# Kernel tuning notes

Hardware: AMD Instinct MI355X
Metric: run time of the kernel (lower is better)

The kernel has to match this reference:

```python
import jax, jax.numpy as jnp
import numpy as np

B, C, V = 1024, 512, 256  # batch, num_conjunctions, num_variables


def setup_inputs() -> dict:
    key = jax.random.key(0)
    k1, k2, k3 = jax.random.split(key, 3)
    x0 = jax.random.uniform(k1, (B, V), dtype=jnp.float32)
    # torch init: conj = 1 - 2*rand  -> uniform in (-1, 1)
    conjunctions = 1.0 - 2.0 * jax.random.uniform(k2, (C, 2 * V), dtype=jnp.float32)
    # rw = 10 - 20*rand -> uniform in (-10, 10)
    rule_weights = 10.0 - 20.0 * jax.random.uniform(k3, (C,), dtype=jnp.float32)
    return {"x0": x0, "conjunctions": conjunctions, "rule_weights": rule_weights}


def reference(x0, conjunctions, rule_weights):
    mu = jax.nn.sigmoid(conjunctions)            # (C, 2V)
    x = jnp.concatenate((x0, 1.0 - x0), axis=1)  # (B, 2V)
    # fuzzy-AND: broadcast mul-add then min over literal axis
    x_pot = mu[None, :, :] * x[:, None, :] + (1.0 - mu)[None, :, :]  # (B, C, 2V)
    fit = jnp.min(x_pot, axis=-1)                # (B, C)
    return 5.0 + jnp.sum(rule_weights * fit, axis=-1)  # (B,)
```

## Files before the change

kernel.cpp:

```cpp
#include <hip/hip_runtime.h>


#define B_    1024
#define C_    512
#define V_    256
#define TWOV  512

#define BPB    8
#define NBG    (B_ / BPB)
#define NCH    2

typedef float    f32x4 __attribute__((ext_vector_type(4)));
typedef _Float16 h16x2 __attribute__((ext_vector_type(2)));

__device__ __forceinline__ float sigf(float z) {
    return 1.0f / (1.0f + __expf(-z));
}
__device__ __forceinline__ float packh2(float a, float b) {
    h16x2 h; h.x = (_Float16)a; h.y = (_Float16)b;
    return __builtin_bit_cast(float, h);
}

#define PKMUL(D, A, Bq) asm("v_pk_mul_f16 %0, %1, %2" : "=v"(D) : "v"(A), "v"(Bq))
#define PKMAX(ACC, T)   asm("v_pk_max_f16 %0, %0, %1" : "+v"(ACC) : "v"(T))

__global__ __launch_bounds__(512) void k_prep(const float* __restrict__ conj,
                                              float4* __restrict__ muH,
                                              float* __restrict__ out) {
    const int vq = blockIdx.x;
    const int c  = threadIdx.x;
    if (vq < 2) out[vq * 512 + c] = 5.0f;
    const float* row = conj + (size_t)c * TWOV;
    const int v = vq * 4;
    float4 r;
    r.x = packh2(sigf(row[v + 0]),      sigf(row[v + 1]));
    r.y = packh2(sigf(row[v + 2]),      sigf(row[v + 3]));
    r.z = packh2(sigf(row[V_ + v + 0]), sigf(row[V_ + v + 1]));
    r.w = packh2(sigf(row[V_ + v + 2]), sigf(row[V_ + v + 3]));
    muH[(size_t)vq * C_ + c] = r;
}

__global__ __launch_bounds__(512, 2) void k_main(const float* __restrict__ x0,
                                                 const float4* __restrict__ muH,
                                                 const float* __restrict__ rw,
                                                 float* __restrict__ out) {
    const int tid  = threadIdx.x;
    const int lane = tid & 63;
    const int wave = tid >> 6;
    const int bg   = blockIdx.x;
    const int chunk= blockIdx.y;
    const int cA   = chunk * 256 + lane;
    const int vq0  = wave * 8;

    __shared__ float4 xs4[BPB * 64];
    __shared__ float  red[8 * 64 * 17];

    {
        const int b = tid >> 6, vq = tid & 63;
        float4 xv = *reinterpret_cast<const float4*>(
            x0 + (size_t)(bg * BPB + b) * V_ + vq * 4);
        float4 pk;
        pk.x = packh2(xv.x, xv.y);
        pk.y = packh2(xv.z, xv.w);
        pk.z = packh2(1.0f - xv.x, 1.0f - xv.y);
        pk.w = packh2(1.0f - xv.z, 1.0f - xv.w);
        xs4[tid] = pk;
    }

    const float4* p = muH + (size_t)vq0 * C_ + cA;

    float accA[BPB], accB[BPB], accC[BPB], accD[BPB];
#pragma unroll
    for (int i = 0; i < BPB; ++i) {
        accA[i] = 0.0f; accB[i] = 0.0f; accC[i] = 0.0f; accD[i] = 0.0f;
    }

    float4 MA = p[0];
    float4 MB = p[64];
    float4 MC = p[128];
    float4 MD = p[192];

    __syncthreads();

#define CPIECE(XC, M, ACC) do { \
    float t0, t1, t2, t3; \
    PKMUL(t0, M.x, XC.z);    \
    PKMUL(t1, M.z, XC.x);    \
    PKMUL(t2, M.y, XC.w);    \
    PKMUL(t3, M.w, XC.y);    \
    PKMAX(ACC, t0); PKMAX(ACC, t1); PKMAX(ACC, t2); PKMAX(ACC, t3); \
    } while (0)

#define PAIR4(XC, bi) do { \
    CPIECE(XC, MA, accA[bi]); \
    CPIECE(XC, MB, accB[bi]); \
    CPIECE(XC, MC, accC[bi]); \
    CPIECE(XC, MD, accD[bi]); \
    } while (0)

#pragma unroll
    for (int q = 0; q < 8; ++q) {
        float4 xc0 = xs4[0 * 64 + vq0 + q];
        float4 xc1 = xs4[1 * 64 + vq0 + q];
        float4 xc2 = xs4[2 * 64 + vq0 + q];
        float4 xc3 = xs4[3 * 64 + vq0 + q];
        float4 xc4 = xs4[4 * 64 + vq0 + q];
        float4 xc5 = xs4[5 * 64 + vq0 + q];
        float4 xc6 = xs4[6 * 64 + vq0 + q];
        float4 xc7 = xs4[7 * 64 + vq0 + q];
        float4 NA, NB, NC, ND;
        if (q < 7) {
            NA = p[(size_t)(q + 1) * C_];
            NB = p[(size_t)(q + 1) * C_ + 64];
            NC = p[(size_t)(q + 1) * C_ + 128];
            ND = p[(size_t)(q + 1) * C_ + 192];
        }
        asm volatile("" : "+v"(MA.x), "+v"(MA.y), "+v"(MA.z), "+v"(MA.w),
                          "+v"(MB.x), "+v"(MB.y), "+v"(MB.z), "+v"(MB.w),
                          "+v"(MC.x), "+v"(MC.y), "+v"(MC.z), "+v"(MC.w),
                          "+v"(MD.x), "+v"(MD.y), "+v"(MD.z), "+v"(MD.w));
        PAIR4(xc0, 0);
        PAIR4(xc1, 1);
        PAIR4(xc2, 2);
        PAIR4(xc3, 3);
        PAIR4(xc4, 4);
        PAIR4(xc5, 5);
        PAIR4(xc6, 6);
        PAIR4(xc7, 7);
        if (q < 7) { MA = NA; MB = NB; MC = NC; MD = ND; }
    }
#undef PAIR4
#undef CPIECE

    float mA[BPB], mB[BPB], mC[BPB], mD[BPB];
#pragma unroll
    for (int bi = 0; bi < BPB; ++bi) {
        h16x2 ha = __builtin_bit_cast(h16x2, accA[bi]);
        h16x2 hb = __builtin_bit_cast(h16x2, accB[bi]);
        h16x2 hc = __builtin_bit_cast(h16x2, accC[bi]);
        h16x2 hd = __builtin_bit_cast(h16x2, accD[bi]);
        mA[bi] = fmaxf((float)ha.x, (float)ha.y);
        mB[bi] = fmaxf((float)hb.x, (float)hb.y);
        mC[bi] = fmaxf((float)hc.x, (float)hc.y);
        mD[bi] = fmaxf((float)hd.x, (float)hd.y);
    }

#define FINROUND(MLO, MHI, COFF) do { \
    _Pragma("unroll") \
    for (int bi = 0; bi < BPB; ++bi) { \
        red[(wave * 64 + lane) * 17 + bi * 2 + 0] = MLO[bi]; \
        red[(wave * 64 + lane) * 17 + bi * 2 + 1] = MHI[bi]; \
    } \
    __syncthreads(); \
    if (wave < 2) { \
        const float rwc = rw[chunk * 256 + (COFF) + wave * 64 + lane]; \
        float con0, con1, con2, con3, con4, con5, con6, con7; \
        FIN(0, con0); FIN(1, con1); FIN(2, con2); FIN(3, con3); \
        FIN(4, con4); FIN(5, con5); FIN(6, con6); FIN(7, con7); \
        float t0 = (lane & 1) ? con1 : con0; \
        float t1 = (lane & 1) ? con3 : con2; \
        float t2 = (lane & 1) ? con5 : con4; \
        float t3 = (lane & 1) ? con7 : con6; \
        float u0 = (lane & 2) ? t1 : t0; \
        float u1 = (lane & 2) ? t3 : t2; \
        float sel = (lane & 4) ? u1 : u0; \
        if (lane < 8) \
            atomicAdd(&out[bg * BPB + lane], sel); \
    } \
    __syncthreads(); \
    } while (0)

#define FIN(bi, CON) do { \
        float mm = red[(0 * 64 + lane) * 17 + (bi) * 2 + wave]; \
        _Pragma("unroll") \
        for (int wv = 1; wv < 8; ++wv) \
            mm = fmaxf(mm, red[(wv * 64 + lane) * 17 + (bi) * 2 + wave]); \
        float v = rwc * (1.0f - mm); \
        v += __shfl_xor(v, 1, 64);  v += __shfl_xor(v, 2, 64); \
        v += __shfl_xor(v, 4, 64);  v += __shfl_xor(v, 8, 64); \
        v += __shfl_xor(v, 16, 64); v += __shfl_xor(v, 32, 64); \
        CON = v; } while (0)

    FINROUND(mA, mB, 0);
    FINROUND(mC, mD, 128);

#undef FIN
#undef FINROUND
}

__global__ __launch_bounds__(256) void k_naive(const float* __restrict__ x0,
                                               const float* __restrict__ conj,
                                               const float* __restrict__ rw,
                                               float* __restrict__ out) {
    int b = blockIdx.x;
    int t = threadIdx.x;
    __shared__ float red[256];
    float acc = 0.0f;
    for (int c = t; c < C_; c += 256) {
        float mm = 0.0f;
        for (int v = 0; v < V_; ++v) {
            float mu1 = 1.0f / (1.0f + expf(-conj[(size_t)c * TWOV + v]));
            float mu2 = 1.0f / (1.0f + expf(-conj[(size_t)c * TWOV + V_ + v]));
            float x = x0[(size_t)b * V_ + v];
            mm = fmaxf(mm, fmaxf(mu1 * (1.0f - x), mu2 * x));
        }
        acc += rw[c] * (1.0f - mm);
    }
    red[t] = acc;
    __syncthreads();
    for (int s = 128; s > 0; s >>= 1) {
        if (t < s) red[t] += red[t + s];
        __syncthreads();
    }
    if (t == 0) out[b] = 5.0f + red[0];
}

extern "C" void kernel_launch(void* const* d_in, const int* in_sizes, int n_in,
                              void* d_out, int out_size, void* d_ws, size_t ws_size,
                              hipStream_t stream) {
    const float* x0   = (const float*)d_in[0];
    const float* conj = (const float*)d_in[1];
    const float* rw   = (const float*)d_in[2];
    float* out = (float*)d_out;

    const size_t need = (size_t)64 * C_ * 16;

    if (ws_size < need) {
        k_naive<<<B_, 256, 0, stream>>>(x0, conj, rw, out);
        return;
    }

    float4* muH = (float4*)d_ws;

    k_prep<<<64, 512, 0, stream>>>(conj, muH, out);
    dim3 grid(NBG, NCH);
    k_main<<<grid, 512, 0, stream>>>(x0, muH, rw, out);
}
```

Before: 22.39 us.

## Halve batch rows per block, raise occupancy, and vectorize prep loads

The main kernel now handles 4 batch rows per block instead of 8. That doubles the grid to 256x2 blocks, and the launch-bounds occupancy hint goes from 2 to 4 blocks per CU. Fewer accumulator registers are needed, but every block reloads the full muH slice, so global/L2 traffic for mu doubles. The prep kernel is reorganised to one block per conjunction with 64 threads, reading each row with coalesced float4 loads instead of strided scalar loads. The final reduction is adapted to 4 rows per block.

```diff
diff --git a/kernel.cpp b/kernel.cpp
--- a/kernel.cpp
+++ b/kernel.cpp
@@ -6,7 +6,7 @@
 #define V_    256
 #define TWOV  512
 
-#define BPB    8
+#define BPB    4
 #define NBG    (B_ / BPB)
 #define NCH    2
 
@@ -24,23 +24,24 @@
 #define PKMUL(D, A, Bq) asm("v_pk_mul_f16 %0, %1, %2" : "=v"(D) : "v"(A), "v"(Bq))
 #define PKMAX(ACC, T)   asm("v_pk_max_f16 %0, %0, %1" : "+v"(ACC) : "v"(T))
 
-__global__ __launch_bounds__(512) void k_prep(const float* __restrict__ conj,
-                                              float4* __restrict__ muH,
-                                              float* __restrict__ out) {
-    const int vq = blockIdx.x;
-    const int c  = threadIdx.x;
-    if (vq < 2) out[vq * 512 + c] = 5.0f;
+__global__ __launch_bounds__(64) void k_prep(const float* __restrict__ conj,
+                                             float4* __restrict__ muH,
+                                             float* __restrict__ out) {
+    const int c  = blockIdx.x;
+    const int vq = threadIdx.x;
+    if (c < 16) out[c * 64 + vq] = 5.0f;
     const float* row = conj + (size_t)c * TWOV;
-    const int v = vq * 4;
+    float4 a = *reinterpret_cast<const float4*>(row + vq * 4);
+    float4 b = *reinterpret_cast<const float4*>(row + V_ + vq * 4);
     float4 r;
-    r.x = packh2(sigf(row[v + 0]),      sigf(row[v + 1]));
-    r.y = packh2(sigf(row[v + 2]),      sigf(row[v + 3]));
-    r.z = packh2(sigf(row[V_ + v + 0]), sigf(row[V_ + v + 1]));
-    r.w = packh2(sigf(row[V_ + v + 2]), sigf(row[V_ + v + 3]));
+    r.x = packh2(sigf(a.x), sigf(a.y));
+    r.y = packh2(sigf(a.z), sigf(a.w));
+    r.z = packh2(sigf(b.x), sigf(b.y));
+    r.w = packh2(sigf(b.z), sigf(b.w));
     muH[(size_t)vq * C_ + c] = r;
 }
 
-__global__ __launch_bounds__(512, 2) void k_main(const float* __restrict__ x0,
+__global__ __launch_bounds__(512, 4) void k_main(const float* __restrict__ x0,
                                                  const float4* __restrict__ muH,
                                                  const float* __restrict__ rw,
                                                  float* __restrict__ out) {
@@ -55,7 +56,7 @@
     __shared__ float4 xs4[BPB * 64];
     __shared__ float  red[8 * 64 * 17];
 
-    {
+    if (tid < BPB * 64) {
         const int b = tid >> 6, vq = tid & 63;
         float4 xv = *reinterpret_cast<const float4*>(
             x0 + (size_t)(bg * BPB + b) * V_ + vq * 4);
@@ -104,10 +105,6 @@
         float4 xc1 = xs4[1 * 64 + vq0 + q];
         float4 xc2 = xs4[2 * 64 + vq0 + q];
         float4 xc3 = xs4[3 * 64 + vq0 + q];
-        float4 xc4 = xs4[4 * 64 + vq0 + q];
-        float4 xc5 = xs4[5 * 64 + vq0 + q];
-        float4 xc6 = xs4[6 * 64 + vq0 + q];
-        float4 xc7 = xs4[7 * 64 + vq0 + q];
         float4 NA, NB, NC, ND;
         if (q < 7) {
             NA = p[(size_t)(q + 1) * C_];
@@ -123,10 +120,6 @@
         PAIR4(xc1, 1);
         PAIR4(xc2, 2);
         PAIR4(xc3, 3);
-        PAIR4(xc4, 4);
-        PAIR4(xc5, 5);
-        PAIR4(xc6, 6);
-        PAIR4(xc7, 7);
         if (q < 7) { MA = NA; MB = NB; MC = NC; MD = ND; }
     }
 #undef PAIR4
@@ -145,31 +138,6 @@
         mD[bi] = fmaxf((float)hd.x, (float)hd.y);
     }
 
-#define FINROUND(MLO, MHI, COFF) do { \
-    _Pragma("unroll") \
-    for (int bi = 0; bi < BPB; ++bi) { \
-        red[(wave * 64 + lane) * 17 + bi * 2 + 0] = MLO[bi]; \
-        red[(wave * 64 + lane) * 17 + bi * 2 + 1] = MHI[bi]; \
-    } \
-    __syncthreads(); \
-    if (wave < 2) { \
-        const float rwc = rw[chunk * 256 + (COFF) + wave * 64 + lane]; \
-        float con0, con1, con2, con3, con4, con5, con6, con7; \
-        FIN(0, con0); FIN(1, con1); FIN(2, con2); FIN(3, con3); \
-        FIN(4, con4); FIN(5, con5); FIN(6, con6); FIN(7, con7); \
-        float t0 = (lane & 1) ? con1 : con0; \
-        float t1 = (lane & 1) ? con3 : con2; \
-        float t2 = (lane & 1) ? con5 : con4; \
-        float t3 = (lane & 1) ? con7 : con6; \
-        float u0 = (lane & 2) ? t1 : t0; \
-        float u1 = (lane & 2) ? t3 : t2; \
-        float sel = (lane & 4) ? u1 : u0; \
-        if (lane < 8) \
-            atomicAdd(&out[bg * BPB + lane], sel); \
-    } \
-    __syncthreads(); \
-    } while (0)
-
 #define FIN(bi, CON) do { \
         float mm = red[(0 * 64 + lane) * 17 + (bi) * 2 + wave]; \
         _Pragma("unroll") \
@@ -181,11 +149,31 @@
         v += __shfl_xor(v, 16, 64); v += __shfl_xor(v, 32, 64); \
         CON = v; } while (0)
 
+#define FINROUND(MLO, MHI, COFF) do { \
+    _Pragma("unroll") \
+    for (int bi = 0; bi < BPB; ++bi) { \
+        red[(wave * 64 + lane) * 17 + bi * 2 + 0] = MLO[bi]; \
+        red[(wave * 64 + lane) * 17 + bi * 2 + 1] = MHI[bi]; \
+    } \
+    __syncthreads(); \
+    if (wave < 2) { \
+        const float rwc = rw[chunk * 256 + (COFF) + wave * 64 + lane]; \
+        float con0, con1, con2, con3; \
+        FIN(0, con0); FIN(1, con1); FIN(2, con2); FIN(3, con3); \
+        float t0 = (lane & 1) ? con1 : con0; \
+        float t1 = (lane & 1) ? con3 : con2; \
+        float sel = (lane & 2) ? t1 : t0; \
+        if (lane < 4) \
+            atomicAdd(&out[bg * BPB + lane], sel); \
+    } \
+    __syncthreads(); \
+    } while (0)
+
     FINROUND(mA, mB, 0);
     FINROUND(mC, mD, 128);
 
+#undef FINROUND
 #undef FIN
-#undef FINROUND
 }
 
 __global__ __launch_bounds__(256) void k_naive(const float* __restrict__ x0,
@@ -232,7 +220,7 @@
 
     float4* muH = (float4*)d_ws;
 
-    k_prep<<<64, 512, 0, stream>>>(conj, muH, out);
+    k_prep<<<C_, 64, 0, stream>>>(conj, muH, out);
     dim3 grid(NBG, NCH);
     k_main<<<grid, 512, 0, stream>>>(x0, muH, rw, out);
 }
```

Measured after the change: 21.58 us. 1.04x faster.
